# Performance work log

Hardware: AMD Instinct MI355X
Metric: run time of the kernel (lower is better)

## Reference

```python
import jax, jax.numpy as jnp
import numpy as np

N = 50000
E = 800000
IN_C, HID, OUT_C = 512, 256, 128


def gcn_conv(x, edge_index, W, b, num_nodes):
    # PyG GCNConv: add self-loops, symmetric normalization, linear-then-aggregate.
    h = x @ W  # [N, out]
    src = jnp.concatenate([edge_index[0], jnp.arange(num_nodes)])
    dst = jnp.concatenate([edge_index[1], jnp.arange(num_nodes)])
    ones = jnp.ones(src.shape[0], dtype=x.dtype)
    deg = jax.ops.segment_sum(ones, dst, num_segments=num_nodes)  # in-degree incl. self-loop
    dinv = jax.lax.rsqrt(deg)  # deg >= 1 thanks to self-loops
    norm = dinv[src] * dinv[dst]  # [E+N]
    msg = h[src] * norm[:, None]  # gather + scale
    out = jax.ops.segment_sum(msg, dst, num_segments=num_nodes)  # scatter-add
    return out + b


def setup_inputs() -> dict:
    key = jax.random.key(0)
    k_x, k_e, k_w1, k_b1, k_w2, k_b2 = jax.random.split(key, 6)
    x = jax.random.normal(k_x, (N, IN_C), dtype=jnp.float32)
    edge_index = jax.random.randint(k_e, (2, E), 0, N, dtype=jnp.int64)
    s1 = 1.0 / np.sqrt(IN_C)
    s2 = 1.0 / np.sqrt(HID)
    W1 = jax.random.uniform(k_w1, (IN_C, HID), jnp.float32, -s1, s1)
    b1 = jax.random.uniform(k_b1, (HID,), jnp.float32, -s1, s1)
    W2 = jax.random.uniform(k_w2, (HID, OUT_C), jnp.float32, -s2, s2)
    b2 = jax.random.uniform(k_b2, (OUT_C,), jnp.float32, -s2, s2)
    return {"x": x, "edge_index": edge_index, "W1": W1, "b1": b1, "W2": W2, "b2": b2}


def reference(x, edge_index, W1, b1, W2, b2):
    h = gcn_conv(x, edge_index, W1, b1, N)
    h = jax.nn.relu(h)
    # dropout in eval mode == identity
    return gcn_conv(h, edge_index, W2, b2, N)
```

## Files before the change

### kernel.cpp

```cpp
#include <hip/hip_runtime.h>
#include <stdint.h>

typedef __bf16 bf16_t;
typedef bf16_t bf16x8 __attribute__((ext_vector_type(8)));
typedef bf16_t bf16x4 __attribute__((ext_vector_type(4)));
typedef bf16_t bf16x2 __attribute__((ext_vector_type(2)));
typedef float  f32x4  __attribute__((ext_vector_type(4)));

#define IN_C 512
#define HID  256
#define OUTC 128

__global__ void k_detect(const void* __restrict__ ei, int* __restrict__ flag, int n_nodes) {
  if (blockIdx.x == 0 && threadIdx.x == 0) {
    const long long* p = (const long long*)ei;
    int ok = 1;
    for (int i = 0; i < 64; ++i) {
      long long v = p[i];
      if (v < 0 || v >= n_nodes) ok = 0;
    }
    *flag = ok;
  }
}

__global__ void k_hist(const void* __restrict__ ei, const int* __restrict__ flag,
                       int* __restrict__ cnt, int E) {
  int e = blockIdx.x * blockDim.x + threadIdx.x;
  if (e >= E) return;
  int d;
  if (*flag) d = (int)((const long long*)ei)[(size_t)E + e];
  else       d = ((const int*)ei)[E + e];
  atomicAdd(&cnt[d], 1);
}

__global__ void k_scan1(const int* __restrict__ cnt, int* __restrict__ ex,
                        int* __restrict__ part, float* __restrict__ dinv, int n) {
  __shared__ int sh[256];
  int i = blockIdx.x * 256 + threadIdx.x;
  int v = (i < n) ? cnt[i] : 0;
  if (i < n) dinv[i] = rsqrtf((float)v + 1.0f);
  sh[threadIdx.x] = v;
  __syncthreads();
  int val = v;
  for (int off = 1; off < 256; off <<= 1) {
    int t = (threadIdx.x >= off) ? sh[threadIdx.x - off] : 0;
    __syncthreads();
    val += t;
    sh[threadIdx.x] = val;
    __syncthreads();
  }
  if (i < n) ex[i] = val - v;
  if (threadIdx.x == 255) part[blockIdx.x] = val;
}

__global__ void k_scan2(int* __restrict__ part, int nb) {
  __shared__ int sh[256];
  int v = (threadIdx.x < nb) ? part[threadIdx.x] : 0;
  sh[threadIdx.x] = v;
  __syncthreads();
  int val = v;
  for (int off = 1; off < 256; off <<= 1) {
    int t = (threadIdx.x >= off) ? sh[threadIdx.x - off] : 0;
    __syncthreads();
    val += t;
    sh[threadIdx.x] = val;
    __syncthreads();
  }
  if (threadIdx.x < nb) part[threadIdx.x] = val - v;
}

__global__ void k_scan3(int* __restrict__ rs, const int* __restrict__ part,
                        int* __restrict__ cur, int n, int Etot) {
  int i = blockIdx.x * 256 + threadIdx.x;
  if (i < n) {
    int r = rs[i] + part[blockIdx.x];
    rs[i] = r;
    cur[i] = r;
  }
  if (i == 0) rs[n] = Etot;
}

__global__ void k_fill(const void* __restrict__ ei, const int* __restrict__ flag,
                       int* __restrict__ cur, int* __restrict__ csr,
                       float* __restrict__ wsrc, const float* __restrict__ dinv, int E) {
  int e = blockIdx.x * blockDim.x + threadIdx.x;
  if (e >= E) return;
  int s, d;
  if (*flag) {
    const long long* p = (const long long*)ei;
    s = (int)p[e];
    d = (int)p[(size_t)E + e];
  } else {
    const int* p = (const int*)ei;
    s = p[e];
    d = p[E + e];
  }
  int pos = atomicAdd(&cur[d], 1);
  csr[pos] = s;
  wsrc[pos] = dinv[s];
}

__global__ void k_transw(const float* __restrict__ W1, const float* __restrict__ W2,
                         bf16_t* __restrict__ W1blk, bf16_t* __restrict__ W2t) {
  int t = blockIdx.x * blockDim.x + threadIdx.x;
  if (t < IN_C * HID) {
    int k = t >> 8, col = t & 255;
    W1blk[(size_t)(k >> 6) * (HID * 64) + col * 64 + (k & 63)] = (bf16_t)W1[t];
  } else {
    int u = t - IN_C * HID;
    if (u < HID * OUTC) {
      int k = u >> 7, col = u & 127;
      W2t[(size_t)col * HID + k] = (bf16_t)W2[u];
    }
  }
}

__global__ __launch_bounds__(256, 2) void k_gemm1(const float* __restrict__ x,
                                                  const bf16_t* __restrict__ Bblk,
                                                  bf16_t* __restrict__ C, int n) {
  __shared__ bf16_t Bs[256 * 72];
  const int bm = blockIdx.x;
  const int tid = threadIdx.x;
  const int wave = tid >> 6, lane = tid & 63;
  const int wm = (wave >> 1) * 32, wn = (wave & 1) * 128;
  const int quad = lane >> 4, l16 = lane & 15;
  const int row0 = bm * 64 + wm + l16;

  f32x4 acc[2][8];
  for (int i = 0; i < 2; ++i)
    for (int j = 0; j < 8; ++j)
      for (int r = 0; r < 4; ++r) acc[i][j][r] = 0.0f;

  for (int kb = 0; kb < 8; ++kb) {
    const int kk = kb * 64;
    bf16x8 afr[2][2];
#pragma unroll
    for (int i = 0; i < 2; ++i) {
      int r = row0 + i * 16;
#pragma unroll
      for (int k2 = 0; k2 < 2; ++k2) {
        if (r < n) {
          const float4* p = (const float4*)(x + (size_t)r * IN_C + kk + k2 * 32 + quad * 8);
          float4 a = p[0], b = p[1];
          afr[i][k2][0] = (bf16_t)a.x; afr[i][k2][1] = (bf16_t)a.y;
          afr[i][k2][2] = (bf16_t)a.z; afr[i][k2][3] = (bf16_t)a.w;
          afr[i][k2][4] = (bf16_t)b.x; afr[i][k2][5] = (bf16_t)b.y;
          afr[i][k2][6] = (bf16_t)b.z; afr[i][k2][7] = (bf16_t)b.w;
        } else {
          for (int u = 0; u < 8; ++u) afr[i][k2][u] = (bf16_t)0.0f;
        }
      }
    }
    __syncthreads();
    const bf16_t* gb = Bblk + (size_t)kb * (HID * 64) + (size_t)tid * 64;
#pragma unroll
    for (int u = 0; u < 8; ++u) {
      bf16x8 v = *(const bf16x8*)(gb + u * 8);
      *(bf16x8*)(&Bs[tid * 72 + u * 8]) = v;
    }
    __syncthreads();
#pragma unroll
    for (int k2 = 0; k2 < 2; ++k2) {
      bf16x8 bfr[8];
#pragma unroll
      for (int j = 0; j < 8; ++j)
        bfr[j] = *(const bf16x8*)(&Bs[(wn + j * 16 + l16) * 72 + k2 * 32 + quad * 8]);
#pragma unroll
      for (int i = 0; i < 2; ++i)
#pragma unroll
        for (int j = 0; j < 8; ++j)
          acc[i][j] = __builtin_amdgcn_mfma_f32_16x16x32_bf16(afr[i][k2], bfr[j], acc[i][j], 0, 0, 0);
    }
  }

#pragma unroll
  for (int i = 0; i < 2; ++i) {
#pragma unroll
    for (int j = 0; j < 8; ++j) {
      int col = wn + j * 16 + l16;
      int rw0 = bm * 64 + wm + i * 16 + quad * 4;
#pragma unroll
      for (int r = 0; r < 4; ++r)
        C[(size_t)(rw0 + r) * HID + col] = (bf16_t)acc[i][j][r];
    }
  }
}

__global__ __launch_bounds__(256, 2) void k_gemm2(const bf16_t* __restrict__ A,
                                                  const bf16_t* __restrict__ W2t,
                                                  bf16_t* __restrict__ C) {
  __shared__ bf16_t Bs[128 * 264];
  const int bm = blockIdx.x;
  const int tid = threadIdx.x;
  const int wave = tid >> 6, lane = tid & 63;
  const int wm = (wave >> 1) * 32, wn = (wave & 1) * 64;
  const int quad = lane >> 4, l16 = lane & 15;

#pragma unroll
  for (int i = 0; i < 16; ++i) {
    int g = i * 256 + tid;
    int row = g >> 5, cc = g & 31;
    bf16x8 v = *(const bf16x8*)(W2t + (size_t)row * HID + cc * 8);
    *(bf16x8*)(&Bs[row * 264 + cc * 8]) = v;
  }
  __syncthreads();

  f32x4 acc[2][4];
  for (int i = 0; i < 2; ++i)
    for (int j = 0; j < 4; ++j)
      for (int r = 0; r < 4; ++r) acc[i][j][r] = 0.0f;

#pragma unroll
  for (int ks = 0; ks < 8; ++ks) {
    const int kk = ks * 32;
    bf16x8 af[2];
#pragma unroll
    for (int i = 0; i < 2; ++i) {
      int r = bm * 64 + wm + i * 16 + l16;
      af[i] = *(const bf16x8*)(A + (size_t)r * HID + kk + quad * 8);
    }
    bf16x8 bfr[4];
#pragma unroll
    for (int j = 0; j < 4; ++j)
      bfr[j] = *(const bf16x8*)(&Bs[(wn + j * 16 + l16) * 264 + kk + quad * 8]);
#pragma unroll
    for (int i = 0; i < 2; ++i)
#pragma unroll
      for (int j = 0; j < 4; ++j)
        acc[i][j] = __builtin_amdgcn_mfma_f32_16x16x32_bf16(af[i], bfr[j], acc[i][j], 0, 0, 0);
  }

#pragma unroll
  for (int i = 0; i < 2; ++i) {
#pragma unroll
    for (int j = 0; j < 4; ++j) {
      int col = wn + j * 16 + l16;
      int rw0 = bm * 64 + wm + i * 16 + quad * 4;
#pragma unroll
      for (int r = 0; r < 4; ++r)
        C[(size_t)(rw0 + r) * OUTC + col] = (bf16_t)acc[i][j][r];
    }
  }
}

__global__ void k_agg_l1(const bf16_t* __restrict__ H, const int* __restrict__ rs,
                         const int* __restrict__ csr, const float* __restrict__ wsrc,
                         const float* __restrict__ dinv, const float* __restrict__ b1,
                         bf16_t* __restrict__ R, int n, int mpad) {
  int d = blockIdx.x * 4 + (threadIdx.x >> 6);
  if (d >= mpad) return;
  int lane = threadIdx.x & 63;
  if (d >= n) {
    bf16x4 z;
    z[0] = (bf16_t)0.0f; z[1] = (bf16_t)0.0f; z[2] = (bf16_t)0.0f; z[3] = (bf16_t)0.0f;
    *(bf16x4*)(R + (size_t)d * HID + lane * 4) = z;
    return;
  }
  int e0 = rs[d], e1 = rs[d + 1];
  float acc[4][4];
  for (int k = 0; k < 4; ++k)
    for (int c = 0; c < 4; ++c) acc[k][c] = 0.f;
  int e = e0;
  for (; e + 8 <= e1; e += 8) {
    int   s[8];
    float w[8];
    bf16x4 h[8];
#pragma unroll
    for (int u = 0; u < 8; ++u) { s[u] = csr[e + u]; w[u] = wsrc[e + u]; }
#pragma unroll
    for (int u = 0; u < 8; ++u)
      h[u] = *(const bf16x4*)(H + (size_t)s[u] * HID + lane * 4);
#pragma unroll
    for (int u = 0; u < 8; ++u)
#pragma unroll
      for (int c = 0; c < 4; ++c) acc[u & 3][c] += w[u] * (float)h[u][c];
  }
  for (; e < e1; ++e) {
    int sx = csr[e];
    float wx = wsrc[e];
    bf16x4 hx = *(const bf16x4*)(H + (size_t)sx * HID + lane * 4);
#pragma unroll
    for (int c = 0; c < 4; ++c) acc[0][c] += wx * (float)hx[c];
  }
  float dd = dinv[d];
  float dv2 = dd * dd;
  bf16x4 hs = *(const bf16x4*)(H + (size_t)d * HID + lane * 4);
  float4 bb = ((const float4*)b1)[lane];
  float a0 = (acc[0][0] + acc[1][0]) + (acc[2][0] + acc[3][0]);
  float a1 = (acc[0][1] + acc[1][1]) + (acc[2][1] + acc[3][1]);
  float a2 = (acc[0][2] + acc[1][2]) + (acc[2][2] + acc[3][2]);
  float a3 = (acc[0][3] + acc[1][3]) + (acc[2][3] + acc[3][3]);
  float v0 = fmaxf(a0 * dd + dv2 * (float)hs[0] + bb.x, 0.f);
  float v1 = fmaxf(a1 * dd + dv2 * (float)hs[1] + bb.y, 0.f);
  float v2 = fmaxf(a2 * dd + dv2 * (float)hs[2] + bb.z, 0.f);
  float v3 = fmaxf(a3 * dd + dv2 * (float)hs[3] + bb.w, 0.f);
  bf16x4 o;
  o[0] = (bf16_t)v0; o[1] = (bf16_t)v1; o[2] = (bf16_t)v2; o[3] = (bf16_t)v3;
  *(bf16x4*)(R + (size_t)d * HID + lane * 4) = o;
}

__global__ void k_agg_l2(const bf16_t* __restrict__ H, const int* __restrict__ rs,
                         const int* __restrict__ csr, const float* __restrict__ wsrc,
                         const float* __restrict__ dinv, const float* __restrict__ b2,
                         float* __restrict__ out, int n) {
  int d = blockIdx.x * 4 + (threadIdx.x >> 6);
  if (d >= n) return;
  int lane = threadIdx.x & 63;
  int e0 = rs[d], e1 = rs[d + 1];
  float acc[4][2];
  for (int k = 0; k < 4; ++k) { acc[k][0] = 0.f; acc[k][1] = 0.f; }
  int e = e0;
  for (; e + 8 <= e1; e += 8) {
    int   s[8];
    float w[8];
    bf16x2 h[8];
#pragma unroll
    for (int u = 0; u < 8; ++u) { s[u] = csr[e + u]; w[u] = wsrc[e + u]; }
#pragma unroll
    for (int u = 0; u < 8; ++u)
      h[u] = *(const bf16x2*)(H + (size_t)s[u] * OUTC + lane * 2);
#pragma unroll
    for (int u = 0; u < 8; ++u) {
      acc[u & 3][0] += w[u] * (float)h[u][0];
      acc[u & 3][1] += w[u] * (float)h[u][1];
    }
  }
  for (; e < e1; ++e) {
    int sx = csr[e];
    float wx = wsrc[e];
    bf16x2 hx = *(const bf16x2*)(H + (size_t)sx * OUTC + lane * 2);
    acc[0][0] += wx * (float)hx[0];
    acc[0][1] += wx * (float)hx[1];
  }
  float a0 = (acc[0][0] + acc[1][0]) + (acc[2][0] + acc[3][0]);
  float a1 = (acc[0][1] + acc[1][1]) + (acc[2][1] + acc[3][1]);
  float dd = dinv[d];
  float dv2 = dd * dd;
  bf16x2 hs = *(const bf16x2*)(H + (size_t)d * OUTC + lane * 2);
  float2 bb = ((const float2*)b2)[lane];
  float2 o;
  o.x = a0 * dd + dv2 * (float)hs[0] + bb.x;
  o.y = a1 * dd + dv2 * (float)hs[1] + bb.y;
  ((float2*)(out + (size_t)d * OUTC))[lane] = o;
}

extern "C" void kernel_launch(void* const* d_in, const int* in_sizes, int n_in,
                              void* d_out, int out_size, void* d_ws, size_t ws_size,
                              hipStream_t stream) {
  const float* x  = (const float*)d_in[0];
  const void*  ei = d_in[1];
  const float* W1 = (const float*)d_in[2];
  const float* b1 = (const float*)d_in[3];
  const float* W2 = (const float*)d_in[4];
  const float* b2 = (const float*)d_in[5];

  const int n = in_sizes[0] / IN_C;
  const int E = in_sizes[1] / 2;
  const int mpad = (n + 63) & ~63;

  char* w = (char*)d_ws;
  size_t off = 0;
  auto alloc = [&](size_t bytes) -> void* {
    void* p = w + off;
    off = (off + bytes + 255) & ~(size_t)255;
    return p;
  };

  int*    flag = (int*)alloc(4);
  int*    cnt  = (int*)alloc((size_t)n * 4);
  float*  dinv = (float*)alloc((size_t)n * 4);
  int*    rs   = (int*)alloc((size_t)(n + 1) * 4);
  int*    cur  = (int*)alloc((size_t)n * 4);
  int*    part = (int*)alloc(1024);
  int*    csr  = (int*)alloc((size_t)E * 4);
  float*  wsrc = (float*)alloc((size_t)E * 4);
  bf16_t* W1blk= (bf16_t*)alloc((size_t)HID * IN_C * 2);
  bf16_t* W2t  = (bf16_t*)alloc((size_t)OUTC * HID * 2);
  bf16_t* H1b  = (bf16_t*)alloc((size_t)mpad * HID * 2);
  bf16_t* R1b  = (bf16_t*)alloc((size_t)mpad * HID * 2);
  bf16_t* H2b  = (bf16_t*)alloc((size_t)mpad * OUTC * 2);
  (void)ws_size; (void)n_in; (void)out_size;

  const int nb = (n + 255) / 256;

  hipMemsetAsync(cnt, 0, (size_t)n * 4, stream);
  k_detect<<<1, 64, 0, stream>>>(ei, flag, n);
  k_hist<<<(E + 255) / 256, 256, 0, stream>>>(ei, flag, cnt, E);
  k_scan1<<<nb, 256, 0, stream>>>(cnt, rs, part, dinv, n);
  k_scan2<<<1, 256, 0, stream>>>(part, nb);
  k_scan3<<<nb, 256, 0, stream>>>(rs, part, cur, n, E);
  k_fill<<<(E + 255) / 256, 256, 0, stream>>>(ei, flag, cur, csr, wsrc, dinv, E);
  k_transw<<<(IN_C * HID + HID * OUTC + 255) / 256, 256, 0, stream>>>(W1, W2, W1blk, W2t);

  k_gemm1<<<mpad / 64, 256, 0, stream>>>(x, W1blk, H1b, n);
  k_agg_l1<<<(mpad + 3) / 4, 256, 0, stream>>>(H1b, rs, csr, wsrc, dinv, b1, R1b, n, mpad);
  k_gemm2<<<mpad / 64, 256, 0, stream>>>(R1b, W2t, H2b);
  k_agg_l2<<<(n + 3) / 4, 256, 0, stream>>>(H2b, rs, csr, wsrc, dinv, b2, (float*)d_out, n);
}
```

Before: 423.6 us.

## Drop LDS staging in GEMMs, prefetch A from global, interleave CSR index and weight

```diff
diff --git a/kernel.cpp b/kernel.cpp
--- a/kernel.cpp
+++ b/kernel.cpp
@@ -10,6 +10,13 @@
 #define IN_C 512
 #define HID  256
 #define OUTC 128
+
+__device__ inline bf16x8 cvt8(float4 a, float4 b) {
+  bf16x8 o;
+  o[0] = (bf16_t)a.x; o[1] = (bf16_t)a.y; o[2] = (bf16_t)a.z; o[3] = (bf16_t)a.w;
+  o[4] = (bf16_t)b.x; o[5] = (bf16_t)b.y; o[6] = (bf16_t)b.z; o[7] = (bf16_t)b.w;
+  return o;
+}
 
 __global__ void k_detect(const void* __restrict__ ei, int* __restrict__ flag, int n_nodes) {
   if (blockIdx.x == 0 && threadIdx.x == 0) {
@@ -81,8 +88,8 @@
 }
 
 __global__ void k_fill(const void* __restrict__ ei, const int* __restrict__ flag,
-                       int* __restrict__ cur, int* __restrict__ csr,
-                       float* __restrict__ wsrc, const float* __restrict__ dinv, int E) {
+                       int* __restrict__ cur, int2* __restrict__ csrw,
+                       const float* __restrict__ dinv, int E) {
   int e = blockIdx.x * blockDim.x + threadIdx.x;
   if (e >= E) return;
   int s, d;
@@ -96,16 +103,18 @@
     d = p[E + e];
   }
   int pos = atomicAdd(&cur[d], 1);
-  csr[pos] = s;
-  wsrc[pos] = dinv[s];
+  int2 v;
+  v.x = s;
+  v.y = __float_as_int(dinv[s]);
+  csrw[pos] = v;
 }
 
 __global__ void k_transw(const float* __restrict__ W1, const float* __restrict__ W2,
-                         bf16_t* __restrict__ W1blk, bf16_t* __restrict__ W2t) {
+                         bf16_t* __restrict__ W1t, bf16_t* __restrict__ W2t) {
   int t = blockIdx.x * blockDim.x + threadIdx.x;
   if (t < IN_C * HID) {
     int k = t >> 8, col = t & 255;
-    W1blk[(size_t)(k >> 6) * (HID * 64) + col * 64 + (k & 63)] = (bf16_t)W1[t];
+    W1t[(size_t)col * IN_C + k] = (bf16_t)W1[t];
   } else {
     int u = t - IN_C * HID;
     if (u < HID * OUTC) {
@@ -116,69 +125,59 @@
 }
 
 __global__ __launch_bounds__(256, 2) void k_gemm1(const float* __restrict__ x,
-                                                  const bf16_t* __restrict__ Bblk,
+                                                  const bf16_t* __restrict__ W1t,
                                                   bf16_t* __restrict__ C, int n) {
-  __shared__ bf16_t Bs[256 * 72];
   const int bm = blockIdx.x;
-  const int tid = threadIdx.x;
-  const int wave = tid >> 6, lane = tid & 63;
-  const int wm = (wave >> 1) * 32, wn = (wave & 1) * 128;
+  const int wv = threadIdx.x >> 6, lane = threadIdx.x & 63;
   const int quad = lane >> 4, l16 = lane & 15;
-  const int row0 = bm * 64 + wm + l16;
-
-  f32x4 acc[2][8];
+  const int r0 = bm * 128 + wv * 32 + l16;
+  const int r1 = r0 + 16;
+  const bool v0 = r0 < n, v1 = r1 < n;
+  const float* p0 = x + (size_t)r0 * IN_C + quad * 8;
+  const float* p1 = x + (size_t)r1 * IN_C + quad * 8;
+  const bf16_t* pb = W1t + (size_t)l16 * IN_C + quad * 8;
+
+  f32x4 acc[2][16];
+#pragma unroll
   for (int i = 0; i < 2; ++i)
-    for (int j = 0; j < 8; ++j)
+#pragma unroll
+    for (int j = 0; j < 16; ++j)
+#pragma unroll
       for (int r = 0; r < 4; ++r) acc[i][j][r] = 0.0f;
 
-  for (int kb = 0; kb < 8; ++kb) {
-    const int kk = kb * 64;
-    bf16x8 afr[2][2];
-#pragma unroll
-    for (int i = 0; i < 2; ++i) {
-      int r = row0 + i * 16;
-#pragma unroll
-      for (int k2 = 0; k2 < 2; ++k2) {
-        if (r < n) {
-          const float4* p = (const float4*)(x + (size_t)r * IN_C + kk + k2 * 32 + quad * 8);
-          float4 a = p[0], b = p[1];
-          afr[i][k2][0] = (bf16_t)a.x; afr[i][k2][1] = (bf16_t)a.y;
-          afr[i][k2][2] = (bf16_t)a.z; afr[i][k2][3] = (bf16_t)a.w;
-          afr[i][k2][4] = (bf16_t)b.x; afr[i][k2][5] = (bf16_t)b.y;
-          afr[i][k2][6] = (bf16_t)b.z; afr[i][k2][7] = (bf16_t)b.w;
-        } else {
-          for (int u = 0; u < 8; ++u) afr[i][k2][u] = (bf16_t)0.0f;
-        }
-      }
-    }
-    __syncthreads();
-    const bf16_t* gb = Bblk + (size_t)kb * (HID * 64) + (size_t)tid * 64;
-#pragma unroll
-    for (int u = 0; u < 8; ++u) {
-      bf16x8 v = *(const bf16x8*)(gb + u * 8);
-      *(bf16x8*)(&Bs[tid * 72 + u * 8]) = v;
-    }
-    __syncthreads();
-#pragma unroll
-    for (int k2 = 0; k2 < 2; ++k2) {
-      bf16x8 bfr[8];
-#pragma unroll
-      for (int j = 0; j < 8; ++j)
-        bfr[j] = *(const bf16x8*)(&Bs[(wn + j * 16 + l16) * 72 + k2 * 32 + quad * 8]);
-#pragma unroll
-      for (int i = 0; i < 2; ++i)
-#pragma unroll
-        for (int j = 0; j < 8; ++j)
-          acc[i][j] = __builtin_amdgcn_mfma_f32_16x16x32_bf16(afr[i][k2], bfr[j], acc[i][j], 0, 0, 0);
-    }
+  float4 A0a, A0b, A1a, A1b;
+  A0a = v0 ? *(const float4*)(p0)     : float4{0, 0, 0, 0};
+  A0b = v0 ? *(const float4*)(p0 + 4) : float4{0, 0, 0, 0};
+  A1a = v1 ? *(const float4*)(p1)     : float4{0, 0, 0, 0};
+  A1b = v1 ? *(const float4*)(p1 + 4) : float4{0, 0, 0, 0};
+
+#pragma unroll
+  for (int kb = 0; kb < 16; ++kb) {
+    float4 N0a, N0b, N1a, N1b;
+    if (kb < 15) {
+      int o = (kb + 1) * 32;
+      N0a = v0 ? *(const float4*)(p0 + o)     : float4{0, 0, 0, 0};
+      N0b = v0 ? *(const float4*)(p0 + o + 4) : float4{0, 0, 0, 0};
+      N1a = v1 ? *(const float4*)(p1 + o)     : float4{0, 0, 0, 0};
+      N1b = v1 ? *(const float4*)(p1 + o + 4) : float4{0, 0, 0, 0};
+    }
+    bf16x8 af0 = cvt8(A0a, A0b);
+    bf16x8 af1 = cvt8(A1a, A1b);
+#pragma unroll
+    for (int j = 0; j < 16; ++j) {
+      bf16x8 bf = *(const bf16x8*)(pb + (size_t)j * 16 * IN_C + kb * 32);
+      acc[0][j] = __builtin_amdgcn_mfma_f32_16x16x32_bf16(af0, bf, acc[0][j], 0, 0, 0);
+      acc[1][j] = __builtin_amdgcn_mfma_f32_16x16x32_bf16(af1, bf, acc[1][j], 0, 0, 0);
+    }
+    A0a = N0a; A0b = N0b; A1a = N1a; A1b = N1b;
   }
 
 #pragma unroll
   for (int i = 0; i < 2; ++i) {
 #pragma unroll
-    for (int j = 0; j < 8; ++j) {
-      int col = wn + j * 16 + l16;
-      int rw0 = bm * 64 + wm + i * 16 + quad * 4;
+    for (int j = 0; j < 16; ++j) {
+      int col = j * 16 + l16;
+      int rw0 = bm * 128 + wv * 32 + i * 16 + quad * 4;
 #pragma unroll
       for (int r = 0; r < 4; ++r)
         C[(size_t)(rw0 + r) * HID + col] = (bf16_t)acc[i][j][r];
@@ -189,53 +188,48 @@
 __global__ __launch_bounds__(256, 2) void k_gemm2(const bf16_t* __restrict__ A,
                                                   const bf16_t* __restrict__ W2t,
                                                   bf16_t* __restrict__ C) {
-  __shared__ bf16_t Bs[128 * 264];
   const int bm = blockIdx.x;
-  const int tid = threadIdx.x;
-  const int wave = tid >> 6, lane = tid & 63;
-  const int wm = (wave >> 1) * 32, wn = (wave & 1) * 64;
+  const int wv = threadIdx.x >> 6, lane = threadIdx.x & 63;
   const int quad = lane >> 4, l16 = lane & 15;
-
-#pragma unroll
-  for (int i = 0; i < 16; ++i) {
-    int g = i * 256 + tid;
-    int row = g >> 5, cc = g & 31;
-    bf16x8 v = *(const bf16x8*)(W2t + (size_t)row * HID + cc * 8);
-    *(bf16x8*)(&Bs[row * 264 + cc * 8]) = v;
-  }
-  __syncthreads();
-
-  f32x4 acc[2][4];
+  const int r0 = bm * 128 + wv * 32 + l16;
+  const int r1 = r0 + 16;
+  const bf16_t* p0 = A + (size_t)r0 * HID + quad * 8;
+  const bf16_t* p1 = A + (size_t)r1 * HID + quad * 8;
+  const bf16_t* pb = W2t + (size_t)l16 * HID + quad * 8;
+
+  f32x4 acc[2][8];
+#pragma unroll
   for (int i = 0; i < 2; ++i)
-    for (int j = 0; j < 4; ++j)
+#pragma unroll
+    for (int j = 0; j < 8; ++j)
+#pragma unroll
       for (int r = 0; r < 4; ++r) acc[i][j][r] = 0.0f;
 
-#pragma unroll
-  for (int ks = 0; ks < 8; ++ks) {
-    const int kk = ks * 32;
-    bf16x8 af[2];
-#pragma unroll
-    for (int i = 0; i < 2; ++i) {
-      int r = bm * 64 + wm + i * 16 + l16;
-      af[i] = *(const bf16x8*)(A + (size_t)r * HID + kk + quad * 8);
-    }
-    bf16x8 bfr[4];
-#pragma unroll
-    for (int j = 0; j < 4; ++j)
-      bfr[j] = *(const bf16x8*)(&Bs[(wn + j * 16 + l16) * 264 + kk + quad * 8]);
-#pragma unroll
-    for (int i = 0; i < 2; ++i)
-#pragma unroll
-      for (int j = 0; j < 4; ++j)
-        acc[i][j] = __builtin_amdgcn_mfma_f32_16x16x32_bf16(af[i], bfr[j], acc[i][j], 0, 0, 0);
+  bf16x8 af0 = *(const bf16x8*)(p0);
+  bf16x8 af1 = *(const bf16x8*)(p1);
+
+#pragma unroll
+  for (int kb = 0; kb < 8; ++kb) {
+    bf16x8 n0, n1;
+    if (kb < 7) {
+      n0 = *(const bf16x8*)(p0 + (kb + 1) * 32);
+      n1 = *(const bf16x8*)(p1 + (kb + 1) * 32);
+    }
+#pragma unroll
+    for (int j = 0; j < 8; ++j) {
+      bf16x8 bf = *(const bf16x8*)(pb + (size_t)j * 16 * HID + kb * 32);
+      acc[0][j] = __builtin_amdgcn_mfma_f32_16x16x32_bf16(af0, bf, acc[0][j], 0, 0, 0);
+      acc[1][j] = __builtin_amdgcn_mfma_f32_16x16x32_bf16(af1, bf, acc[1][j], 0, 0, 0);
+    }
+    af0 = n0; af1 = n1;
   }
 
 #pragma unroll
   for (int i = 0; i < 2; ++i) {
 #pragma unroll
-    for (int j = 0; j < 4; ++j) {
-      int col = wn + j * 16 + l16;
-      int rw0 = bm * 64 + wm + i * 16 + quad * 4;
+    for (int j = 0; j < 8; ++j) {
+      int col = j * 16 + l16;
+      int rw0 = bm * 128 + wv * 32 + i * 16 + quad * 4;
 #pragma unroll
       for (int r = 0; r < 4; ++r)
         C[(size_t)(rw0 + r) * OUTC + col] = (bf16_t)acc[i][j][r];
@@ -244,9 +238,9 @@
 }
 
 __global__ void k_agg_l1(const bf16_t* __restrict__ H, const int* __restrict__ rs,
-                         const int* __restrict__ csr, const float* __restrict__ wsrc,
-                         const float* __restrict__ dinv, const float* __restrict__ b1,
-                         bf16_t* __restrict__ R, int n, int mpad) {
+                         const int2* __restrict__ csrw, const float* __restrict__ dinv,
+                         const float* __restrict__ b1, bf16_t* __restrict__ R,
+                         int n, int mpad) {
   int d = blockIdx.x * 4 + (threadIdx.x >> 6);
   if (d >= mpad) return;
   int lane = threadIdx.x & 63;
@@ -262,25 +256,26 @@
     for (int c = 0; c < 4; ++c) acc[k][c] = 0.f;
   int e = e0;
   for (; e + 8 <= e1; e += 8) {
-    int   s[8];
-    float w[8];
+    int2 cw[8];
     bf16x4 h[8];
 #pragma unroll
-    for (int u = 0; u < 8; ++u) { s[u] = csr[e + u]; w[u] = wsrc[e + u]; }
+    for (int u = 0; u < 8; ++u) cw[u] = csrw[e + u];
 #pragma unroll
     for (int u = 0; u < 8; ++u)
-      h[u] = *(const bf16x4*)(H + (size_t)s[u] * HID + lane * 4);
-#pragma unroll
-    for (int u = 0; u < 8; ++u)
-#pragma unroll
-      for (int c = 0; c < 4; ++c) acc[u & 3][c] += w[u] * (float)h[u][c];
+      h[u] = *(const bf16x4*)(H + (size_t)cw[u].x * HID + lane * 4);
+#pragma unroll
+    for (int u = 0; u < 8; ++u) {
+      float w = __int_as_float(cw[u].y);
+#pragma unroll
+      for (int c = 0; c < 4; ++c) acc[u & 3][c] += w * (float)h[u][c];
+    }
   }
   for (; e < e1; ++e) {
-    int sx = csr[e];
-    float wx = wsrc[e];
-    bf16x4 hx = *(const bf16x4*)(H + (size_t)sx * HID + lane * 4);
-#pragma unroll
-    for (int c = 0; c < 4; ++c) acc[0][c] += wx * (float)hx[c];
+    int2 cw = csrw[e];
+    float w = __int_as_float(cw.y);
+    bf16x4 hx = *(const bf16x4*)(H + (size_t)cw.x * HID + lane * 4);
+#pragma unroll
+    for (int c = 0; c < 4; ++c) acc[0][c] += w * (float)hx[c];
   }
   float dd = dinv[d];
   float dv2 = dd * dd;
@@ -300,9 +295,8 @@
 }
 
 __global__ void k_agg_l2(const bf16_t* __restrict__ H, const int* __restrict__ rs,
-                         const int* __restrict__ csr, const float* __restrict__ wsrc,
-                         const float* __restrict__ dinv, const float* __restrict__ b2,
-                         float* __restrict__ out, int n) {
+                         const int2* __restrict__ csrw, const float* __restrict__ dinv,
+                         const float* __restrict__ b2, float* __restrict__ out, int n) {
   int d = blockIdx.x * 4 + (threadIdx.x >> 6);
   if (d >= n) return;
   int lane = threadIdx.x & 63;
@@ -311,26 +305,26 @@
   for (int k = 0; k < 4; ++k) { acc[k][0] = 0.f; acc[k][1] = 0.f; }
   int e = e0;
   for (; e + 8 <= e1; e += 8) {
-    int   s[8];
-    float w[8];
+    int2 cw[8];
     bf16x2 h[8];
 #pragma unroll
-    for (int u = 0; u < 8; ++u) { s[u] = csr[e + u]; w[u] = wsrc[e + u]; }
+    for (int u = 0; u < 8; ++u) cw[u] = csrw[e + u];
 #pragma unroll
     for (int u = 0; u < 8; ++u)
-      h[u] = *(const bf16x2*)(H + (size_t)s[u] * OUTC + lane * 2);
+      h[u] = *(const bf16x2*)(H + (size_t)cw[u].x * OUTC + lane * 2);
 #pragma unroll
     for (int u = 0; u < 8; ++u) {
-      acc[u & 3][0] += w[u] * (float)h[u][0];
-      acc[u & 3][1] += w[u] * (float)h[u][1];
+      float w = __int_as_float(cw[u].y);
+      acc[u & 3][0] += w * (float)h[u][0];
+      acc[u & 3][1] += w * (float)h[u][1];
     }
   }
   for (; e < e1; ++e) {
-    int sx = csr[e];
-    float wx = wsrc[e];
-    bf16x2 hx = *(const bf16x2*)(H + (size_t)sx * OUTC + lane * 2);
-    acc[0][0] += wx * (float)hx[0];
-    acc[0][1] += wx * (float)hx[1];
+    int2 cw = csrw[e];
+    float w = __int_as_float(cw.y);
+    bf16x2 hx = *(const bf16x2*)(H + (size_t)cw.x * OUTC + lane * 2);
+    acc[0][0] += w * (float)hx[0];
+    acc[0][1] += w * (float)hx[1];
   }
   float a0 = (acc[0][0] + acc[1][0]) + (acc[2][0] + acc[3][0]);
   float a1 = (acc[0][1] + acc[1][1]) + (acc[2][1] + acc[3][1]);
@@ -356,7 +350,7 @@
 
   const int n = in_sizes[0] / IN_C;
   const int E = in_sizes[1] / 2;
-  const int mpad = (n + 63) & ~63;
+  const int mpad = (n + 127) & ~127;
 
   char* w = (char*)d_ws;
   size_t off = 0;
@@ -372,9 +366,8 @@
   int*    rs   = (int*)alloc((size_t)(n + 1) * 4);
   int*    cur  = (int*)alloc((size_t)n * 4);
   int*    part = (int*)alloc(1024);
-  int*    csr  = (int*)alloc((size_t)E * 4);
-  float*  wsrc = (float*)alloc((size_t)E * 4);
-  bf16_t* W1blk= (bf16_t*)alloc((size_t)HID * IN_C * 2);
+  int2*   csrw = (int2*)alloc((size_t)E * 8);
+  bf16_t* W1t  = (bf16_t*)alloc((size_t)HID * IN_C * 2);
   bf16_t* W2t  = (bf16_t*)alloc((size_t)OUTC * HID * 2);
   bf16_t* H1b  = (bf16_t*)alloc((size_t)mpad * HID * 2);
   bf16_t* R1b  = (bf16_t*)alloc((size_t)mpad * HID * 2);
@@ -389,11 +382,11 @@
   k_scan1<<<nb, 256, 0, stream>>>(cnt, rs, part, dinv, n);
   k_scan2<<<1, 256, 0, stream>>>(part, nb);
   k_scan3<<<nb, 256, 0, stream>>>(rs, part, cur, n, E);
-  k_fill<<<(E + 255) / 256, 256, 0, stream>>>(ei, flag, cur, csr, wsrc, dinv, E);
-  k_transw<<<(IN_C * HID + HID * OUTC + 255) / 256, 256, 0, stream>>>(W1, W2, W1blk, W2t);
-
-  k_gemm1<<<mpad / 64, 256, 0, stream>>>(x, W1blk, H1b, n);
-  k_agg_l1<<<(mpad + 3) / 4, 256, 0, stream>>>(H1b, rs, csr, wsrc, dinv, b1, R1b, n, mpad);
-  k_gemm2<<<mpad / 64, 256, 0, stream>>>(R1b, W2t, H2b);
-  k_agg_l2<<<(n + 3) / 4, 256, 0, stream>>>(H2b, rs, csr, wsrc, dinv, b2, (float*)d_out, n);
-}
+  k_fill<<<(E + 255) / 256, 256, 0, stream>>>(ei, flag, cur, csrw, dinv, E);
+  k_transw<<<(IN_C * HID + HID * OUTC + 255) / 256, 256, 0, stream>>>(W1, W2, W1t, W2t);
+
+  k_gemm1<<<mpad / 128, 256, 0, stream>>>(x, W1t, H1b, n);
+  k_agg_l1<<<(mpad + 3) / 4, 256, 0, stream>>>(H1b, rs, csrw, dinv, b1, R1b, n, mpad);
+  k_gemm2<<<mpad / 128, 256, 0, stream>>>(R1b, W2t, H2b);
+  k_agg_l2<<<(n + 3) / 4, 256, 0, stream>>>(H2b, rs, csrw, dinv, b2, (float*)d_out, n);
+}
```

Result: slower. 436.6 us (+3.1%).
